# Performance work log

Hardware: AMD Instinct MI355X
Metric: run time of the kernel (lower is better)

## Reference

```python
import jax, jax.numpy as jnp
import numpy as np

NH = 12          # num attention heads
EPS = 1e-6       # layer-norm eps
B, T_, S_, H, E, IE = 8, 8, 196, 768, 4, 768  # IE = intermediate_size // num_experts


def layernorm(x, g, b):
    m = jnp.mean(x, axis=-1, keepdims=True)
    v = jnp.var(x, axis=-1, keepdims=True)
    return (x - m) / jnp.sqrt(v + EPS) * g + b


def mha(x, qkv_w, qkv_b, proj_w, proj_b):
    # x: [B', N, H]
    Bp, N, Hh = x.shape
    hd = Hh // NH
    qkv = (x @ qkv_w + qkv_b).reshape(Bp, N, 3, NH, hd).transpose(2, 0, 3, 1, 4)
    q, k, v = qkv[0], qkv[1], qkv[2]                      # [B', nh, N, hd]
    attn = jax.nn.softmax(jnp.einsum('bhqd,bhkd->bhqk', q, k) * (hd ** -0.5), axis=-1)
    out = jnp.einsum('bhqk,bhkd->bhqd', attn, v).transpose(0, 2, 1, 3).reshape(Bp, N, Hh)
    return out @ proj_w + proj_b


def moe_mlp(x, gate_up, down, eids):
    # x: [B, N, H]; gate_up: [E, H, 2*IE]; down: [E, IE, H]; eids: [N]
    sel = jax.nn.one_hot(eids, gate_up.shape[0], dtype=x.dtype)  # [N, E]
    gu = jnp.einsum('bnh,ehk,ne->bnk', x, gate_up, sel)          # per-token expert gate+up
    gate, up = gu[..., :IE], gu[..., IE:]
    inter = jax.nn.silu(gate) * up                               # SwiGLU
    return jnp.einsum('bni,eih,ne->bnh', inter, down, sel)


def setup_inputs() -> dict:
    key = jax.random.key(0)
    ks = jax.random.split(key, 16)
    w = lambda k, shp: (jax.random.normal(k, shp, dtype=jnp.float32) * 0.02)
    inp = {
        'x': jax.random.normal(ks[0], (B, T_ * S_, H), dtype=jnp.float32),
        'qkv_w_s': w(ks[1], (H, 3 * H)), 'qkv_b_s': jnp.zeros((3 * H,), jnp.float32),
        'proj_w_s': w(ks[2], (H, H)),    'proj_b_s': jnp.zeros((H,), jnp.float32),
        'qkv_w_t': w(ks[3], (H, 3 * H)), 'qkv_b_t': jnp.zeros((3 * H,), jnp.float32),
        'proj_w_t': w(ks[4], (H, H)),    'proj_b_t': jnp.zeros((H,), jnp.float32),
        'ln_s_g': jnp.ones((H,), jnp.float32), 'ln_s_b': jnp.zeros((H,), jnp.float32),
        'ln_t_g': jnp.ones((H,), jnp.float32), 'ln_t_b': jnp.zeros((H,), jnp.float32),
        'ln_m_g': jnp.ones((H,), jnp.float32), 'ln_m_b': jnp.zeros((H,), jnp.float32),
        'gate_up_proj': w(ks[5], (E, H, 2 * IE)),
        'down_proj': w(ks[6], (E, IE, H)),
        'T': T_, 'S': S_,
        'expert_ids': jax.random.randint(ks[7], (T_ * S_,), 0, E, dtype=jnp.int32),
    }
    return inp


def reference(x, qkv_w_s, qkv_b_s, proj_w_s, proj_b_s,
              qkv_w_t, qkv_b_t, proj_w_t, proj_b_t,
              ln_s_g, ln_s_b, ln_t_g, ln_t_b, ln_m_g, ln_m_b,
              gate_up_proj, down_proj, T, S, expert_ids):
    Bb, N, Hh = x.shape
    # 1) spatial attention over S patches within each of B*T frames
    xs = layernorm(x, ln_s_g, ln_s_b).reshape(Bb * T, S, Hh)
    xs = mha(xs, qkv_w_s, qkv_b_s, proj_w_s, proj_b_s).reshape(Bb, T * S, Hh)
    x = x + xs
    # 2) temporal attention over T frames at each of B*S spatial positions
    xt = layernorm(x, ln_t_g, ln_t_b).reshape(Bb, T, S, Hh).transpose(0, 2, 1, 3).reshape(Bb * S, T, Hh)
    xt = mha(xt, qkv_w_t, qkv_b_t, proj_w_t, proj_b_t)
    xt = xt.reshape(Bb, S, T, Hh).transpose(0, 2, 1, 3).reshape(Bb, T * S, Hh)
    x = x + xt
    # 3) token-routed MoE MLP
    x = x + moe_mlp(layernorm(x, ln_m_g, ln_m_b), gate_up_proj, down_proj, expert_ids)
    return x
```

## Files before the change

### kernel.cpp

```cpp
#include <hip/hip_runtime.h>

typedef __bf16 bf16;
typedef bf16 bf16x8 __attribute__((ext_vector_type(8)));
typedef float f32x4 __attribute__((ext_vector_type(4)));

#define BB 8
#define TT 8
#define SS 196
#define NTOK 1568
#define ROWS 12544
#define HH 768
#define HD 64

__device__ __forceinline__ void gload16(const void* g, void* l) {
  __builtin_amdgcn_global_load_lds(
      (const __attribute__((address_space(1))) void*)g,
      (__attribute__((address_space(3))) void*)l, 16, 0, 0);
}

__global__ __launch_bounds__(256)
void transpose_w(const float* __restrict__ in, bf16* __restrict__ out, int K, int N) {
  in  += (size_t)blockIdx.z * K * N;
  out += (size_t)blockIdx.z * K * N;
  __shared__ float tile[64][65];
  const int k0 = blockIdx.x * 64, n0 = blockIdx.y * 64;
  const int tx = threadIdx.x & 63, ty = threadIdx.x >> 6;
  #pragma unroll
  for (int rr = ty; rr < 64; rr += 4)
    tile[rr][tx] = in[(size_t)(k0 + rr) * N + n0 + tx];
  __syncthreads();
  #pragma unroll
  for (int rr = ty; rr < 64; rr += 4)
    out[(size_t)(n0 + rr) * K + k0 + tx] = (bf16)tile[tx][rr];
}

__global__ __launch_bounds__(256)
void transpose_gu(const float* __restrict__ in, bf16* __restrict__ out) {
  const int K = 768, N = 1536;
  in  += (size_t)blockIdx.z * K * N;
  out += (size_t)blockIdx.z * K * N;
  __shared__ float tile[64][65];
  const int k0 = blockIdx.x * 64, n0 = blockIdx.y * 64;
  const int tx = threadIdx.x & 63, ty = threadIdx.x >> 6;
  const int s = n0 >> 6;
  #pragma unroll
  for (int rr = ty; rr < 64; rr += 4) {
    const int src = (tx < 32) ? (s * 32 + tx) : (768 + s * 32 + tx - 32);
    tile[rr][tx] = in[(size_t)(k0 + rr) * N + src];
  }
  __syncthreads();
  #pragma unroll
  for (int rr = ty; rr < 64; rr += 4)
    out[(size_t)(n0 + rr) * K + k0 + tx] = (bf16)tile[tx][rr];
}

__global__ __launch_bounds__(256)
void ln_kernel(const float* __restrict__ x, const float* __restrict__ g,
               const float* __restrict__ b, bf16* __restrict__ out) {
  const int row = blockIdx.x * 4 + (threadIdx.x >> 6);
  const int lane = threadIdx.x & 63;
  const float* xr = x + (size_t)row * HH;
  float v[12];
  float sum = 0.f, sq = 0.f;
  #pragma unroll
  for (int i = 0; i < 12; ++i) {
    v[i] = xr[lane + i * 64];
    sum += v[i];
    sq += v[i] * v[i];
  }
  #pragma unroll
  for (int off = 32; off > 0; off >>= 1) {
    sum += __shfl_xor(sum, off);
    sq  += __shfl_xor(sq, off);
  }
  const float mean = sum * (1.f / 768.f);
  const float var = sq * (1.f / 768.f) - mean * mean;
  const float inv = rsqrtf(var + 1e-6f);
  bf16* op = out + (size_t)row * HH;
  #pragma unroll
  for (int i = 0; i < 12; ++i) {
    const int c = lane + i * 64;
    op[c] = (bf16)((v[i] - mean) * inv * g[c] + b[c]);
  }
}

template<bool MOE, bool BIAS, bool RESID, bool OBF16, bool GUFUSE>
__global__ __launch_bounds__(256, 2)
void gemmDP(const bf16* __restrict__ A, const bf16* __restrict__ BT,
            const float* __restrict__ bias, const float* __restrict__ resid,
            float* __restrict__ outF, bf16* __restrict__ outB,
            int N, int K, int NMT,
            const int* __restrict__ perm, const int4* __restrict__ descs,
            const int* __restrict__ meta) {
  __shared__ __align__(16) bf16 lds[4 * 8192];
  __shared__ int rowLds[128];

  const int tid = threadIdx.x;
  const int G = gridDim.x;
  int work;
  {
    const int q = G >> 3, r = G & 7, xcd = blockIdx.x & 7, pos = blockIdx.x >> 3;
    work = (xcd < r ? xcd * (q + 1) : r * (q + 1) + (xcd - r) * q) + pos;
  }
  int M0 = 0, N0, ncnt = 16;
  if constexpr (MOE) {
    const int ntile = work % NMT, desc = work / NMT;
    if (desc >= meta[0]) return;
    int4 d = descs[desc];
    BT += (size_t)d.x * N * K;
    ncnt = d.z;
    N0 = ntile * 128;
    if (tid < 128) {
      const int nl = tid >> 3, b = tid & 7;
      const int n = perm[d.y + (nl < ncnt ? nl : ncnt - 1)];
      rowLds[tid] = b * NTOK + n;
    }
    __syncthreads();
  } else {
    const int mt = work % NMT, nt = work / NMT;
    M0 = mt * 128;
    N0 = nt * 128;
  }

  const int w = tid >> 6, lane = tid & 63;
  const int wr = w >> 1, wc = w & 1;
  const int lr = lane & 15, lg = lane >> 4;

  const int r0 = tid >> 2;
  const int sseg = ((tid & 3) ^ ((tid >> 3) & 3)) * 8;
  int arow0, arow1;
  if constexpr (MOE) {
    arow0 = rowLds[r0];
    arow1 = rowLds[64 + r0];
  } else {
    arow0 = M0 + r0;
    arow1 = M0 + 64 + r0;
  }
  const bf16* aP0 = A + (size_t)arow0 * K + sseg;
  const bf16* aP1 = A + (size_t)arow1 * K + sseg;
  const bf16* bP0 = BT + (size_t)(N0 + r0) * K + sseg;
  const bf16* bP1 = BT + (size_t)(N0 + 64 + r0) * K + sseg;

  auto STG = [&](int kt) {
    bf16* buf = lds + (kt & 3) * 8192;
    const int ko = kt << 5;
    gload16(aP0 + ko, buf + tid * 8);
    gload16(aP1 + ko, buf + 2048 + tid * 8);
    gload16(bP0 + ko, buf + 4096 + tid * 8);
    gload16(bP1 + ko, buf + 6144 + tid * 8);
  };

  const int axr = (lg ^ ((lr >> 1) & 3)) * 8;

  f32x4 acc[4][4] = {};
  const int NT = K >> 5;

  STG(0); STG(1); STG(2);

  for (int t = 0; t < NT; ++t) {
    if (t + 2 < NT)      { asm volatile("s_waitcnt vmcnt(8)" ::: "memory"); }
    else if (t + 1 < NT) { asm volatile("s_waitcnt vmcnt(4)" ::: "memory"); }
    else                 { asm volatile("s_waitcnt vmcnt(0)" ::: "memory"); }
    __builtin_amdgcn_s_barrier();
    asm volatile("" ::: "memory");

    const bf16* Ab = lds + (t & 3) * 8192;
    const bf16* Bb = Ab + 4096;
    bf16x8 a[4], b[4];
    #pragma unroll
    for (int mf = 0; mf < 4; ++mf) {
      const int row = wr * 64 + mf * 16 + lr;
      a[mf] = *(const bf16x8*)(Ab + row * 32 + axr);
    }
    #pragma unroll
    for (int nf = 0; nf < 4; ++nf) {
      const int row = wc * 64 + nf * 16 + lr;
      b[nf] = *(const bf16x8*)(Bb + row * 32 + axr);
    }
    if (t + 3 < NT) STG(t + 3);

    asm volatile("s_waitcnt lgkmcnt(0)" ::: "memory");
    __builtin_amdgcn_sched_barrier(0);
    __builtin_amdgcn_s_setprio(1);
    #pragma unroll
    for (int mf = 0; mf < 4; ++mf)
      #pragma unroll
      for (int nf = 0; nf < 4; ++nf)
        acc[mf][nf] = __builtin_amdgcn_mfma_f32_16x16x32_bf16(a[mf], b[nf], acc[mf][nf], 0, 0, 0);
    __builtin_amdgcn_s_setprio(0);
    asm volatile("" ::: "memory");
  }

  #pragma unroll
  for (int m = 0; m < 4; ++m) {
    #pragma unroll
    for (int j = 0; j < 4; ++j) {
      const int r = wr * 64 + m * 16 + lg * 4 + j;
      if (MOE && ((r >> 3) >= ncnt)) continue;
      const size_t grow = MOE ? (size_t)rowLds[r] : (size_t)(M0 + r);
      if constexpr (GUFUSE) {
        const size_t rbase = grow * 768;
        #pragma unroll
        for (int n = 0; n < 2; ++n) {
          const int icol = (N0 >> 1) + wc * 32 + n * 16 + lr;
          const float g = acc[m][n][j], u = acc[m][n + 2][j];
          outB[rbase + icol] = (bf16)(g / (1.f + __expf(-g)) * u);
        }
      } else {
        const size_t rbase = grow * N;
        #pragma unroll
        for (int n = 0; n < 4; ++n) {
          const int gcol = N0 + wc * 64 + n * 16 + lr;
          float v = acc[m][n][j];
          if constexpr (BIAS)  v += bias[gcol];
          if constexpr (RESID) v += resid[rbase + gcol];
          if constexpr (OBF16) outB[rbase + gcol] = (bf16)v;
          else                 outF[rbase + gcol] = v;
        }
      }
    }
  }
}

#define SPAD 208
#define VST 232
__global__ __launch_bounds__(512)
void attn_spatial(const bf16* __restrict__ qkv, bf16* __restrict__ out) {
  __shared__ __align__(16) bf16 Ks[SPAD * 64];
  __shared__ __align__(16) bf16 Vt[64 * VST];
  __shared__ __align__(16) bf16 Pb[8][16 * VST];

  const int bp = blockIdx.x, h = blockIdx.y;
  const int tid = threadIdx.x;
  const int w = tid >> 6, lane = tid & 63;
  const int lr = lane & 15, lg = lane >> 4;
  const size_t base = (size_t)bp * SS * 2304 + h * HD;

  for (int cb = w * 64; cb < SPAD * 8; cb += 512) {
    const int c = cb + lane;
    const int row = c >> 3, seg = c & 7;
    const int srow = row < SS ? row : SS - 1;
    const int sseg = seg ^ (row & 7);
    gload16(qkv + base + (size_t)srow * 2304 + 768 + sseg * 8, Ks + cb * 8);
  }
  for (int t = tid; t < 224 * 8; t += 512) {
    const int k = t >> 3, dseg = t & 7;
    const int sk = k < SS ? k : SS - 1;
    bf16x8 v = *(const bf16x8*)(qkv + base + (size_t)sk * 2304 + 1536 + dseg * 8);
    #pragma unroll
    for (int i = 0; i < 8; ++i) Vt[(dseg * 8 + i) * VST + k] = v[i];
  }
  bf16* Pw = Pb[w];
  for (int i = lane; i < 256; i += 64)
    Pw[(i >> 4) * VST + 208 + (i & 15)] = (bf16)0.f;
  __syncthreads();

  for (int t = w; t < 13; t += 8) {
    const int q0 = t * 16;
    const int qr = q0 + lr;
    const bf16* qp = qkv + base + (size_t)(qr < SS ? qr : SS - 1) * 2304 + lg * 8;
    const bf16x8 af0 = *(const bf16x8*)qp;
    const bf16x8 af1 = *(const bf16x8*)(qp + 32);

    f32x4 sc[13];
    #pragma unroll
    for (int f = 0; f < 13; ++f) sc[f] = (f32x4){0.f, 0.f, 0.f, 0.f};
    #pragma unroll
    for (int f = 0; f < 13; ++f) {
      const int key = f * 16 + lr;
      const bf16x8 bv0 = *(const bf16x8*)&Ks[key * 64 + ((lg) ^ (key & 7)) * 8];
      const bf16x8 bv1 = *(const bf16x8*)&Ks[key * 64 + ((4 + lg) ^ (key & 7)) * 8];
      sc[f] = __builtin_amdgcn_mfma_f32_16x16x32_bf16(af0, bv0, sc[f], 0, 0, 0);
      sc[f] = __builtin_amdgcn_mfma_f32_16x16x32_bf16(af1, bv1, sc[f], 0, 0, 0);
    }
    #pragma unroll
    for (int f = 0; f < 13; ++f)
      #pragma unroll
      for (int j = 0; j < 4; ++j) sc[f][j] *= 0.125f;
    if (192 + lr >= SS)
      #pragma unroll
      for (int j = 0; j < 4; ++j) sc[12][j] = -1e30f;

    float mx[4], ls[4];
    #pragma unroll
    for (int j = 0; j < 4; ++j) {
      float m = sc[0][j];
      #pragma unroll
      for (int f = 1; f < 13; ++f) m = fmaxf(m, sc[f][j]);
      #pragma unroll
      for (int off = 1; off < 16; off <<= 1) m = fmaxf(m, __shfl_xor(m, off));
      mx[j] = m;
    }
    #pragma unroll
    for (int j = 0; j < 4; ++j) ls[j] = 0.f;
    #pragma unroll
    for (int f = 0; f < 13; ++f) {
      #pragma unroll
      for (int j = 0; j < 4; ++j) {
        const float p = __expf(sc[f][j] - mx[j]);
        ls[j] += p;
        Pw[(lg * 4 + j) * VST + f * 16 + lr] = (bf16)p;
      }
    }
    #pragma unroll
    for (int j = 0; j < 4; ++j) {
      #pragma unroll
      for (int off = 1; off < 16; off <<= 1) ls[j] += __shfl_xor(ls[j], off);
      ls[j] = 1.f / ls[j];
    }

    f32x4 oacc[4];
    #pragma unroll
    for (int n = 0; n < 4; ++n) oacc[n] = (f32x4){0.f, 0.f, 0.f, 0.f};
    #pragma unroll
    for (int kb = 0; kb < 7; ++kb) {
      const bf16x8 pa = *(const bf16x8*)&Pw[lr * VST + kb * 32 + lg * 8];
      #pragma unroll
      for (int n = 0; n < 4; ++n) {
        const bf16x8 bv = *(const bf16x8*)&Vt[(n * 16 + lr) * VST + kb * 32 + lg * 8];
        oacc[n] = __builtin_amdgcn_mfma_f32_16x16x32_bf16(pa, bv, oacc[n], 0, 0, 0);
      }
    }
    #pragma unroll
    for (int j = 0; j < 4; ++j) {
      const int row = q0 + lg * 4 + j;
      if (row < SS) {
        bf16* op = out + ((size_t)bp * SS + row) * 768 + h * HD;
        #pragma unroll
        for (int n = 0; n < 4; ++n) op[n * 16 + lr] = (bf16)(oacc[n][j] * ls[j]);
      }
    }
  }
}

__global__ __launch_bounds__(256)
void attn_temporal(const bf16* __restrict__ qkv, bf16* __restrict__ out) {
  const int pair = blockIdx.x * 4 + (threadIdx.x >> 6);
  const int lane = threadIdx.x & 63;
  const int h = pair % 12;
  const int bs = pair / 12;
  const int b = bs / SS, s = bs - b * SS;
  const size_t row0 = (size_t)b * NTOK + s;
  const int q = lane >> 3, k = lane & 7;
  const bf16* qr = qkv + (row0 + (size_t)q * SS) * 2304 + h * HD;
  const bf16* kr = qkv + (row0 + (size_t)k * SS) * 2304 + 768 + h * HD;
  float sc = 0.f;
  #pragma unroll
  for (int j = 0; j < 8; ++j) {
    bf16x8 qv = ((const bf16x8*)qr)[j];
    bf16x8 kv = ((const bf16x8*)kr)[j];
    #pragma unroll
    for (int d = 0; d < 8; ++d) sc += (float)qv[d] * (float)kv[d];
  }
  sc *= 0.125f;
  float mxv = sc;
  #pragma unroll
  for (int off = 1; off < 8; off <<= 1) mxv = fmaxf(mxv, __shfl_xor(mxv, off));
  float p = __expf(sc - mxv);
  float sum = p;
  #pragma unroll
  for (int off = 1; off < 8; off <<= 1) sum += __shfl_xor(sum, off);
  p /= sum;

  const int dg = lane & 7;
  float o[8] = {0, 0, 0, 0, 0, 0, 0, 0};
  #pragma unroll
  for (int kk = 0; kk < 8; ++kk) {
    const float pk = __shfl(p, (lane & 56) + kk);
    const bf16* vr = qkv + (row0 + (size_t)kk * SS) * 2304 + 1536 + h * HD + dg * 8;
    bf16x8 vv = *(const bf16x8*)vr;
    #pragma unroll
    for (int j = 0; j < 8; ++j) o[j] += pk * (float)vv[j];
  }
  bf16* op = out + (row0 + (size_t)q * SS) * 768 + h * HD + dg * 8;
  bf16x8 ov;
  #pragma unroll
  for (int j = 0; j < 8; ++j) ov[j] = (bf16)o[j];
  *(bf16x8*)op = ov;
}

__global__ __launch_bounds__(256)
void sort_moe(const int* __restrict__ eids, int* __restrict__ perm,
              int4* __restrict__ descs, int* __restrict__ meta) {
  __shared__ int cnt[4], base[4], cur[4];
  const int tid = threadIdx.x;
  if (tid < 4) cnt[tid] = 0;
  __syncthreads();
  for (int n = tid; n < NTOK; n += 256) atomicAdd(&cnt[eids[n]], 1);
  __syncthreads();
  if (tid == 0) {
    int off = 0;
    for (int e = 0; e < 4; ++e) { base[e] = off; cur[e] = off; off += cnt[e]; }
  }
  __syncthreads();
  for (int n = tid; n < NTOK; n += 256) {
    const int pos = atomicAdd(&cur[eids[n]], 1);
    perm[pos] = n;
  }
  if (tid == 0) {
    int t = 0;
    for (int e = 0; e < 4; ++e)
      for (int st = 0; st < cnt[e]; st += 16) {
        const int c = cnt[e] - st;
        descs[t++] = make_int4(e, base[e] + st, c < 16 ? c : 16, 0);
      }
    meta[0] = t;
  }
}

extern "C" void kernel_launch(void* const* d_in, const int* in_sizes, int n_in,
                              void* d_out, int out_size, void* d_ws, size_t ws_size,
                              hipStream_t stream) {
  (void)in_sizes; (void)n_in; (void)out_size; (void)ws_size;
  const float* x        = (const float*)d_in[0];
  const float* qkv_w_s  = (const float*)d_in[1];
  const float* qkv_b_s  = (const float*)d_in[2];
  const float* proj_w_s = (const float*)d_in[3];
  const float* proj_b_s = (const float*)d_in[4];
  const float* qkv_w_t  = (const float*)d_in[5];
  const float* qkv_b_t  = (const float*)d_in[6];
  const float* proj_w_t = (const float*)d_in[7];
  const float* proj_b_t = (const float*)d_in[8];
  const float* ln_s_g   = (const float*)d_in[9];
  const float* ln_s_b   = (const float*)d_in[10];
  const float* ln_t_g   = (const float*)d_in[11];
  const float* ln_t_b   = (const float*)d_in[12];
  const float* ln_m_g   = (const float*)d_in[13];
  const float* ln_m_b   = (const float*)d_in[14];
  const float* gate_up  = (const float*)d_in[15];
  const float* down_w   = (const float*)d_in[16];
  const int* expert_ids = (const int*)d_in[19];
  float* out = (float*)d_out;

  char* ws = (char*)d_ws;
  bf16* qkvsT   = (bf16*)(ws + 0);
  bf16* projsT  = (bf16*)(ws + 3538944);
  bf16* qkvtT   = (bf16*)(ws + 4718592);
  bf16* projtT  = (bf16*)(ws + 8257536);
  bf16* guT     = (bf16*)(ws + 9437184);
  bf16* downT   = (bf16*)(ws + 18874368);
  bf16* lnbuf   = (bf16*)(ws + 23592960);
  bf16* qkvbuf  = (bf16*)(ws + 42860544);
  bf16* attnbuf = (bf16*)(ws + 100663296);
  float* x1     = (float*)(ws + 119930880);
  int*  perm    = (int*)(ws + 158466048);
  int4* descs   = (int4*)(ws + 158472320);
  int*  meta    = (int*)(ws + 158473952);

  const dim3 blk(256);
  const dim3 blk512(512);

  transpose_w<<<dim3(12, 36, 1), blk, 0, stream>>>(qkv_w_s, qkvsT, 768, 2304);
  transpose_w<<<dim3(12, 12, 1), blk, 0, stream>>>(proj_w_s, projsT, 768, 768);
  transpose_w<<<dim3(12, 36, 1), blk, 0, stream>>>(qkv_w_t, qkvtT, 768, 2304);
  transpose_w<<<dim3(12, 12, 1), blk, 0, stream>>>(proj_w_t, projtT, 768, 768);
  transpose_gu<<<dim3(12, 24, 4), blk, 0, stream>>>(gate_up, guT);
  transpose_w<<<dim3(12, 12, 4), blk, 0, stream>>>(down_w, downT, 768, 768);

  ln_kernel<<<3136, blk, 0, stream>>>(x, ln_s_g, ln_s_b, lnbuf);
  gemmDP<false, true, false, true, false><<<dim3(98 * 18), blk, 0, stream>>>(
      lnbuf, qkvsT, qkv_b_s, nullptr, nullptr, qkvbuf, 2304, 768, 98,
      nullptr, nullptr, nullptr);
  attn_spatial<<<dim3(64, 12), blk512, 0, stream>>>(qkvbuf, attnbuf);
  gemmDP<false, true, true, false, false><<<dim3(98 * 6), blk, 0, stream>>>(
      attnbuf, projsT, proj_b_s, x, x1, nullptr, 768, 768, 98,
      nullptr, nullptr, nullptr);

  ln_kernel<<<3136, blk, 0, stream>>>(x1, ln_t_g, ln_t_b, lnbuf);
  gemmDP<false, true, false, true, false><<<dim3(98 * 18), blk, 0, stream>>>(
      lnbuf, qkvtT, qkv_b_t, nullptr, nullptr, qkvbuf, 2304, 768, 98,
      nullptr, nullptr, nullptr);
  attn_temporal<<<4704, blk, 0, stream>>>(qkvbuf, attnbuf);
  gemmDP<false, true, true, false, false><<<dim3(98 * 6), blk, 0, stream>>>(
      attnbuf, projtT, proj_b_t, x1, out, nullptr, 768, 768, 98,
      nullptr, nullptr, nullptr);

  ln_kernel<<<3136, blk, 0, stream>>>(out, ln_m_g, ln_m_b, lnbuf);
  sort_moe<<<1, blk, 0, stream>>>(expert_ids, perm, descs, meta);
  gemmDP<true, false, false, true, true><<<dim3(12 * 102), blk, 0, stream>>>(
      lnbuf, guT, nullptr, nullptr, nullptr, qkvbuf, 1536, 768, 12,
      perm, descs, meta);
  gemmDP<true, false, true, false, false><<<dim3(6 * 102), blk, 0, stream>>>(
      qkvbuf, downT, nullptr, out, out, nullptr, 768, 768, 6,
      perm, descs, meta);
}
```

Before: 435.2 us.

## Store intermediate residual in bf16 and swap GEMM tile ordering to row-major

The intermediate residual x1 after spatial attention is now stored as bf16 instead of fp32. The temporal layernorm and the temporal proj residual add read it as bf16, which halves that buffer's write and read traffic. Separately, the dense GEMM work mapping now iterates N tiles fastest within an M tile, so consecutive blocks share A rows rather than B columns. The bf16 residual loses precision in the skip path and may increase error against the fp32 reference.

```diff
diff --git a/kernel.cpp b/kernel.cpp
--- a/kernel.cpp
+++ b/kernel.cpp
@@ -54,17 +54,18 @@
     out[(size_t)(n0 + rr) * K + k0 + tx] = (bf16)tile[tx][rr];
 }
 
+template<typename TI>
 __global__ __launch_bounds__(256)
-void ln_kernel(const float* __restrict__ x, const float* __restrict__ g,
+void ln_kernel(const TI* __restrict__ x, const float* __restrict__ g,
                const float* __restrict__ b, bf16* __restrict__ out) {
   const int row = blockIdx.x * 4 + (threadIdx.x >> 6);
   const int lane = threadIdx.x & 63;
-  const float* xr = x + (size_t)row * HH;
+  const TI* xr = x + (size_t)row * HH;
   float v[12];
   float sum = 0.f, sq = 0.f;
   #pragma unroll
   for (int i = 0; i < 12; ++i) {
-    v[i] = xr[lane + i * 64];
+    v[i] = (float)xr[lane + i * 64];
     sum += v[i];
     sq += v[i] * v[i];
   }
@@ -84,10 +85,10 @@
   }
 }
 
-template<bool MOE, bool BIAS, bool RESID, bool OBF16, bool GUFUSE>
+template<bool MOE, bool BIAS, bool RESID, bool RB16, bool OBF16, bool GUFUSE>
 __global__ __launch_bounds__(256, 2)
 void gemmDP(const bf16* __restrict__ A, const bf16* __restrict__ BT,
-            const float* __restrict__ bias, const float* __restrict__ resid,
+            const float* __restrict__ bias, const void* __restrict__ resid,
             float* __restrict__ outF, bf16* __restrict__ outB,
             int N, int K, int NMT,
             const int* __restrict__ perm, const int4* __restrict__ descs,
@@ -117,7 +118,7 @@
     }
     __syncthreads();
   } else {
-    const int mt = work % NMT, nt = work / NMT;
+    const int mt = work / NMT, nt = work % NMT;
     M0 = mt * 128;
     N0 = nt * 128;
   }
@@ -213,7 +214,10 @@
           const int gcol = N0 + wc * 64 + n * 16 + lr;
           float v = acc[m][n][j];
           if constexpr (BIAS)  v += bias[gcol];
-          if constexpr (RESID) v += resid[rbase + gcol];
+          if constexpr (RESID) {
+            if constexpr (RB16) v += (float)((const bf16*)resid)[rbase + gcol];
+            else                v += ((const float*)resid)[rbase + gcol];
+          }
           if constexpr (OBF16) outB[rbase + gcol] = (bf16)v;
           else                 outF[rbase + gcol] = v;
         }
@@ -442,7 +446,7 @@
   bf16* lnbuf   = (bf16*)(ws + 23592960);
   bf16* qkvbuf  = (bf16*)(ws + 42860544);
   bf16* attnbuf = (bf16*)(ws + 100663296);
-  float* x1     = (float*)(ws + 119930880);
+  bf16* x1b     = (bf16*)(ws + 119930880);
   int*  perm    = (int*)(ws + 158466048);
   int4* descs   = (int4*)(ws + 158472320);
   int*  meta    = (int*)(ws + 158473952);
@@ -457,30 +461,30 @@
   transpose_gu<<<dim3(12, 24, 4), blk, 0, stream>>>(gate_up, guT);
   transpose_w<<<dim3(12, 12, 4), blk, 0, stream>>>(down_w, downT, 768, 768);
 
-  ln_kernel<<<3136, blk, 0, stream>>>(x, ln_s_g, ln_s_b, lnbuf);
-  gemmDP<false, true, false, true, false><<<dim3(98 * 18), blk, 0, stream>>>(
-      lnbuf, qkvsT, qkv_b_s, nullptr, nullptr, qkvbuf, 2304, 768, 98,
+  ln_kernel<float><<<3136, blk, 0, stream>>>(x, ln_s_g, ln_s_b, lnbuf);
+  gemmDP<false, true, false, false, true, false><<<dim3(98 * 18), blk, 0, stream>>>(
+      lnbuf, qkvsT, qkv_b_s, nullptr, nullptr, qkvbuf, 2304, 768, 18,
       nullptr, nullptr, nullptr);
   attn_spatial<<<dim3(64, 12), blk512, 0, stream>>>(qkvbuf, attnbuf);
-  gemmDP<false, true, true, false, false><<<dim3(98 * 6), blk, 0, stream>>>(
-      attnbuf, projsT, proj_b_s, x, x1, nullptr, 768, 768, 98,
+  gemmDP<false, true, true, false, true, false><<<dim3(98 * 6), blk, 0, stream>>>(
+      attnbuf, projsT, proj_b_s, x, nullptr, x1b, 768, 768, 6,
       nullptr, nullptr, nullptr);
 
-  ln_kernel<<<3136, blk, 0, stream>>>(x1, ln_t_g, ln_t_b, lnbuf);
-  gemmDP<false, true, false, true, false><<<dim3(98 * 18), blk, 0, stream>>>(
-      lnbuf, qkvtT, qkv_b_t, nullptr, nullptr, qkvbuf, 2304, 768, 98,
+  ln_kernel<bf16><<<3136, blk, 0, stream>>>(x1b, ln_t_g, ln_t_b, lnbuf);
+  gemmDP<false, true, false, false, true, false><<<dim3(98 * 18), blk, 0, stream>>>(
+      lnbuf, qkvtT, qkv_b_t, nullptr, nullptr, qkvbuf, 2304, 768, 18,
       nullptr, nullptr, nullptr);
   attn_temporal<<<4704, blk, 0, stream>>>(qkvbuf, attnbuf);
-  gemmDP<false, true, true, false, false><<<dim3(98 * 6), blk, 0, stream>>>(
-      attnbuf, projtT, proj_b_t, x1, out, nullptr, 768, 768, 98,
+  gemmDP<false, true, true, true, false, false><<<dim3(98 * 6), blk, 0, stream>>>(
+      attnbuf, projtT, proj_b_t, x1b, out, nullptr, 768, 768, 6,
       nullptr, nullptr, nullptr);
 
-  ln_kernel<<<3136, blk, 0, stream>>>(out, ln_m_g, ln_m_b, lnbuf);
+  ln_kernel<float><<<3136, blk, 0, stream>>>(out, ln_m_g, ln_m_b, lnbuf);
   sort_moe<<<1, blk, 0, stream>>>(expert_ids, perm, descs, meta);
-  gemmDP<true, false, false, true, true><<<dim3(12 * 102), blk, 0, stream>>>(
+  gemmDP<true, false, false, false, true, true><<<dim3(12 * 102), blk, 0, stream>>>(
       lnbuf, guT, nullptr, nullptr, nullptr, qkvbuf, 1536, 768, 12,
       perm, descs, meta);
-  gemmDP<true, false, true, false, false><<<dim3(6 * 102), blk, 0, stream>>>(
+  gemmDP<true, false, true, false, false, false><<<dim3(6 * 102), blk, 0, stream>>>(
       qkvbuf, downT, nullptr, out, out, nullptr, 768, 768, 6,
       perm, descs, meta);
 }
```

Result: faster. 400.5 us (-8.0%).
